# Kernel optimization log

Hardware: AMD Instinct MI355X
Metric: run time of the kernel (lower is better)

The kernel has to match this reference:

```python
import jax, jax.numpy as jnp
import numpy as np

B, S, DIN, E, M, L = 16, 4096, 64, 512, 128, 4


def _phi(u, R):
    # u: [B,S,E] (already scaled by E**-0.25), R: [E,M]
    logits = u @ R - 0.5 * jnp.sum(u * u, axis=-1, keepdims=True)
    logits = logits - jax.lax.stop_gradient(jnp.max(logits))  # constant shift cancels in num/den ratio
    return jnp.exp(logits) / np.sqrt(M).astype(np.float32)


def setup_inputs() -> dict:
    key = jax.random.key(0)
    ks = jax.random.split(key, 32)
    n = jax.random.normal
    d = {
        'x': n(ks[0], (B, S, DIN), jnp.float32),
        'Wi': n(ks[1], (DIN, E)) / np.sqrt(DIN),
        'bi': jnp.zeros((E,)),
        'pos': n(ks[2], (S, E)) * 0.02,
        'Wq': n(ks[3], (L, E, E)) / np.sqrt(E),
        'bq': jnp.zeros((L, E)),
        'Wk': n(ks[4], (L, E, E)) / np.sqrt(E),
        'bk': jnp.zeros((L, E)),
        'Wv': n(ks[5], (L, E, E)) / np.sqrt(E),
        'bv': jnp.zeros((L, E)),
        'Wo': n(ks[6], (L, E, E)) / np.sqrt(E),
        'bo': jnp.zeros((L, E)),
        'R': n(ks[7], (L, E, M)),
        'ln_g': jnp.ones((L, E)),
        'ln_b': jnp.zeros((L, E)),
        'W1': n(ks[8], (L, E, 4 * E)) / np.sqrt(E),
        'b1': jnp.zeros((L, 4 * E)),
        'W2': n(ks[9], (L, 4 * E, E)) / np.sqrt(4 * E),
        'b2': jnp.zeros((L, E)),
        'Wr1': n(ks[10], (E, E // 2)) / np.sqrt(E),
        'br1': jnp.zeros((E // 2,)),
        'Wr2': n(ks[11], (E // 2, 1)) / np.sqrt(E // 2),
        'br2': jnp.zeros((1,)),
    }
    return d


def reference(x, Wi, bi, pos, Wq, bq, Wk, bk, Wv, bv, Wo, bo, R, ln_g, ln_b, W1, b1, W2, b2, Wr1, br1, Wr2, br2):
    h = x @ Wi + bi + pos[None, :, :]  # [B,S,E]
    scale = E ** -0.25
    for i in range(L):
        residual = h
        # --- Performer linear attention (non-causal FAVOR+) ---
        q = h @ Wq[i] + bq[i]
        k = h @ Wk[i] + bk[i]
        v = h @ Wv[i] + bv[i]
        pq = _phi(q * scale, R[i])  # [B,S,M]
        pk = _phi(k * scale, R[i])  # [B,S,M]
        kv = jnp.einsum('bsm,bse->bme', pk, v)  # [B,M,E]
        z = jnp.sum(pk, axis=1)                  # [B,M]
        num = jnp.einsum('bsm,bme->bse', pq, kv)
        den = jnp.einsum('bsm,bm->bs', pq, z)[..., None]
        a = (num / (den + 1e-6)) @ Wo[i] + bo[i]
        # --- LayerNorm ---
        mu = jnp.mean(a, axis=-1, keepdims=True)
        var = jnp.var(a, axis=-1, keepdims=True)
        y = (a - mu) * jax.lax.rsqrt(var + 1e-5) * ln_g[i] + ln_b[i]
        # --- FFN (dropout is identity in eval) ---
        ff = jax.nn.gelu(y @ W1[i] + b1[i], approximate=False) @ W2[i] + b2[i]
        h = ff + residual
    pooled = h[:, 0, :]  # [B,E]
    return jax.nn.relu(pooled @ Wr1 + br1) @ Wr2 + br2  # [B,1]
```

## Files before the change

### kernel.cpp

```cpp
#include <hip/hip_runtime.h>
#include <math.h>

static constexpr int  cB   = 16;
static constexpr int  cS   = 4096;
static constexpr int  cDIN = 64;
static constexpr int  cE   = 512;
static constexpr int  cM   = 128;
static constexpr int  cL   = 4;
static constexpr int  cFF  = 2048;
static constexpr int  cHE  = 256;
static constexpr long cNBS = (long)cB * cS;
static constexpr int  cNF  = 1536;

typedef __attribute__((ext_vector_type(8))) short  bf16x8;
typedef __attribute__((ext_vector_type(4))) short  bf16x4;
typedef __attribute__((ext_vector_type(4))) float  f32x4;

typedef const __attribute__((address_space(1))) unsigned int g_u32;
typedef __attribute__((address_space(3))) unsigned int l_u32;

__device__ __forceinline__ float b2f(unsigned short u) {
  union { unsigned int i; float f; } x; x.i = ((unsigned int)u) << 16; return x.f;
}
__device__ __forceinline__ unsigned short f2b(float f) {
  union { float f; unsigned int i; } x; x.f = f;
  unsigned int r = x.i + 0x7FFFu + ((x.i >> 16) & 1u);
  return (unsigned short)(r >> 16);
}

#define PSCALE 0.21022410381342863f
#define PNRM   0.022097086912079608f
#define PINV   0.08838834764831845f

#define FLAG_BIAS    2
#define FLAG_GELU    4
#define FLAG_RES     8
#define FLAG_VT      16
#define FLAG_DEN     32
#define FLAG_RNORM   64
#define FLAG_PHIK    128
#define FLAG_F32OUT  256
#define FLAG_SPLITK8 512
#define FLAG_ATOMIC  1024
#define FLAG_FUSED   2048
#define FLAG_SWZ     4096

#define GMT 128
#define GNT 128
#define GBK 64


__global__ __launch_bounds__(256, 2)
void gemm_kernel(const unsigned short* __restrict__ A,
                 const unsigned short* __restrict__ Bt,
                 const unsigned short* __restrict__ bias,
                 const unsigned short* __restrict__ Res,
                 const float* __restrict__ aux,
                 float* __restrict__ pmax,
                 void* __restrict__ C,
                 int K, int N, int lda, int ldb, float alpha, int flags,
                 long sA, long sB, long sC)
{
  __shared__ __align__(16) unsigned char sraw[32800];
  unsigned short (*As)[64] = (unsigned short (*)[64])sraw;
  unsigned short (*Bs)[64] = (unsigned short (*)[64])(sraw + 16384);
  unsigned short (*stage)[136] = (unsigned short (*)[136])sraw;
  float* wred  = (float*)(sraw + 32768);

  const int tid  = threadIdx.x;
  const int lane = tid & 63;
  const int wid  = tid >> 6;

  int bx = blockIdx.x, by = blockIdx.y;
  if (flags & FLAG_SWZ) {
    const unsigned lid  = blockIdx.x + gridDim.x * blockIdx.y;
    const unsigned xcd  = lid & 7u;
    const unsigned slot = lid >> 3;
    bx = (int)(xcd * (gridDim.y >> 3) + slot / gridDim.x);
    by = (int)(slot % gridDim.x);
  }

  long zb = blockIdx.z;
  const long zc = blockIdx.z;
  int koff = 0;
  if (flags & FLAG_SPLITK8) { koff = (int)(zb & 7) * K; zb >>= 3; }

  const unsigned short* Ab = A + zb * sA + (long)bx * GMT * lda + koff;
  const unsigned short* Bb = Bt + zb * sB + (long)by * GNT * ldb + koff;

  const int srow  = tid >> 3;
  const int scolG = (((tid & 7) ^ (srow & 7)) << 3);
  const unsigned short* gA = Ab + (long)srow * lda + scolG;
  const unsigned short* gB = Bb + (long)srow * ldb + scolG;
  l_u32* lA = (l_u32*)(sraw + tid * 16);
  l_u32* lB = (l_u32*)(sraw + 16384 + tid * 16);

  const f32x4 fzero = {0.f, 0.f, 0.f, 0.f};
  f32x4 acc[4][4];
#pragma unroll
  for (int i = 0; i < 4; ++i)
#pragma unroll
    for (int j = 0; j < 4; ++j) acc[i][j] = fzero;

  const int wm = (wid >> 1) << 6;
  const int wn = (wid & 1) << 6;
  const int fm = lane & 15;
  const int kqh = lane >> 4;

  const long ka32 = (long)32 * lda, kb32 = (long)32 * ldb;
  for (int k0 = 0; k0 < K; k0 += GBK) {
#pragma unroll
    for (int s = 0; s < 4; ++s) {
      __builtin_amdgcn_global_load_lds((g_u32*)(gA + (long)s * ka32 + k0),
                                       (l_u32*)((__attribute__((address_space(3))) char*)lA + s * 4096), 16, 0, 0);
      __builtin_amdgcn_global_load_lds((g_u32*)(gB + (long)s * kb32 + k0),
                                       (l_u32*)((__attribute__((address_space(3))) char*)lB + s * 4096), 16, 0, 0);
    }
    __syncthreads();

#pragma unroll
    for (int kk = 0; kk < 2; ++kk) {
      bf16x8 af[4], bfv[4];
#pragma unroll
      for (int i = 0; i < 4; ++i) {
        const int ca = ((((kk << 2) | kqh) ^ (fm & 7)) << 3);
        af[i]  = *(const bf16x8*)&As[wm + i * 16 + fm][ca];
        bfv[i] = *(const bf16x8*)&Bs[wn + i * 16 + fm][ca];
      }
#pragma unroll
      for (int i = 0; i < 4; ++i)
#pragma unroll
        for (int j = 0; j < 4; ++j)
          acc[i][j] = __builtin_amdgcn_mfma_f32_16x16x32_bf16(af[i], bfv[j], acc[i][j], 0, 0, 0);
    }
    __syncthreads();
  }

  const int rq = (lane >> 4) << 2;
  const long crow0 = (long)bx * GMT + wm;
  const int  ccol0 = by * GNT + wn;

  long rnoff = 0;
  if (flags & FLAG_FUSED) {
    if (by < 4) flags = FLAG_BIAS | FLAG_VT;
    else { flags = FLAG_BIAS | FLAG_RNORM; if (by >= 8) rnoff = cNBS; }
  }

  if (flags & FLAG_RNORM) {
#pragma unroll
    for (int i = 0; i < 4; ++i)
#pragma unroll
      for (int r = 0; r < 4; ++r) {
        float s = 0.f;
#pragma unroll
        for (int j = 0; j < 4; ++j) {
          float v = acc[i][j][r] * alpha + b2f(bias[ccol0 + j * 16 + fm]);
          s += v * v;
        }
        s += __shfl_xor(s, 1, 64);
        s += __shfl_xor(s, 2, 64);
        s += __shfl_xor(s, 4, 64);
        s += __shfl_xor(s, 8, 64);
        if (fm == 0)
          unsafeAtomicAdd(&pmax[rnoff + crow0 + i * 16 + rq + r], s);
      }
    return;
  }

  if (flags & FLAG_PHIK) {
    const long aoff = (by == 0) ? cNBS : 0;
    float* Cf = (float*)C + (long)by * (cNBS * (long)cM);
    float mx = -3.0e38f;
#pragma unroll
    for (int i = 0; i < 4; ++i)
#pragma unroll
      for (int r = 0; r < 4; ++r) {
        const long rr = crow0 + i * 16 + rq + r;
        const float nrm = PNRM * aux[aoff + rr];
#pragma unroll
        for (int j = 0; j < 4; ++j) {
          const int cc = ccol0 + j * 16 + fm;
          const float bv = b2f(bias[cc]);
          float l = acc[i][j][r] * PSCALE + bv - nrm;
          mx = fmaxf(mx, l);
          Cf[rr * (long)cM + (cc & (cM - 1))] = l;
        }
      }
#pragma unroll
    for (int off = 32; off >= 1; off >>= 1) mx = fmaxf(mx, __shfl_down(mx, off, 64));
    if (lane == 0) wred[wid] = mx;
    __syncthreads();
    if (tid == 0)
      pmax[by * 512 + bx] = fmaxf(fmaxf(wred[0], wred[1]), fmaxf(wred[2], wred[3]));
    return;
  }

  if (flags & FLAG_ATOMIC) {
    float* Cf = (float*)C + zb * sC;
#pragma unroll
    for (int j = 0; j < 4; ++j) {
      const int cc = ccol0 + j * 16 + fm;
#pragma unroll
      for (int i = 0; i < 4; ++i)
#pragma unroll
        for (int r = 0; r < 4; ++r) {
          const long rr = crow0 + i * 16 + rq + r;
          unsafeAtomicAdd(&Cf[rr * (long)N + cc], acc[i][j][r] * alpha);
        }
    }
    return;
  }

  if (flags & FLAG_VT) {
    unsigned short* Cb = (unsigned short*)C;
    const int bb = (bx * GMT) >> 12;
    const long sbase = (long)((bx * GMT) & (cS - 1));
#pragma unroll
    for (int rnd = 0; rnd < 2; ++rnd) {
      if ((wn >> 6) == rnd) {
#pragma unroll
        for (int j = 0; j < 4; ++j) {
          const int cc = ccol0 + j * 16 + fm;
          const float bv = (flags & FLAG_BIAS) ? b2f(bias[cc]) : 0.f;
          const int cl = j * 16 + fm;
#pragma unroll
          for (int i = 0; i < 4; ++i)
#pragma unroll
            for (int r = 0; r < 4; ++r)
              stage[cl][wm + i * 16 + rq + r] = f2b(acc[i][j][r] * alpha + bv);
        }
      }
      __syncthreads();
      {
        const int cl = tid >> 2;
        const int sseg = (tid & 3) << 5;
        const int gcol = by * GNT + rnd * 64 + cl;
        unsigned short* dst = Cb + (long)bb * sC + (long)gcol * cS + sbase + sseg;
#pragma unroll
        for (int t = 0; t < 4; ++t)
          *(bf16x8*)(dst + t * 8) = *(const bf16x8*)&stage[cl][sseg + t * 8];
      }
      __syncthreads();
    }
    return;
  }

  const long rowsPerBatch = (long)gridDim.x * GMT;
#pragma unroll
  for (int j = 0; j < 4; ++j) {
    const int cc = ccol0 + j * 16 + fm;
    const float bv = (flags & FLAG_BIAS) ? b2f(bias[cc]) : 0.f;
#pragma unroll
    for (int i = 0; i < 4; ++i) {
      const long rbase = crow0 + i * 16 + rq;
#pragma unroll
      for (int r = 0; r < 4; ++r) {
        const long rr = rbase + r;
        float v = acc[i][j][r] * alpha;
        if (flags & FLAG_DEN)
          v *= 1.f / (fmaxf(aux[zb * rowsPerBatch + rr], 0.f) + 1e-6f);
        v += bv;
        if (flags & FLAG_GELU) v = 0.5f * v * (1.f + erff(v * 0.7071067811865475f));
        const long idx = zc * sC + rr * (long)N + cc;
        if (flags & FLAG_RES) v += b2f(Res[idx]);
        if (flags & FLAG_F32OUT) ((float*)C)[idx] = v;
        else                     ((unsigned short*)C)[idx] = f2b(v);
      }
    }
  }
}

__global__ void detect_kernel(const unsigned short* __restrict__ lng,
                              int* __restrict__ flag) {
  if (threadIdx.x == 0 && blockIdx.x == 0) flag[0] = (lng[0] == 0) ? 1 : 0;
}

__global__ __launch_bounds__(256) void cvt_kernel(const void* __restrict__ in,
                                                  unsigned short* __restrict__ out,
                                                  long n, const int* __restrict__ flag) {
  long i = (long)blockIdx.x * 256 + threadIdx.x;
  if (i >= n) return;
  if (flag[0]) out[i] = f2b(((const float*)in)[i]);
  else         out[i] = ((const unsigned short*)in)[i];
}

__global__ __launch_bounds__(256) void zero4_kernel(float* __restrict__ p) {
  long i = ((long)blockIdx.x * 256 + threadIdx.x) * 4;
  f32x4 z = {0.f, 0.f, 0.f, 0.f};
  *(f32x4*)&p[i] = z;
}

__global__ __launch_bounds__(256) void addpos_kernel(unsigned short* __restrict__ h,
                                                     const unsigned short* __restrict__ pos) {
  long i = ((long)blockIdx.x * 256 + threadIdx.x) * 8;
  long se = i % ((long)cS * cE);
  bf16x8 v = *(bf16x8*)&h[i];
  bf16x8 p = *(const bf16x8*)&pos[se];
#pragma unroll
  for (int r = 0; r < 8; ++r)
    v[r] = (short)f2b(b2f((unsigned short)v[r]) + b2f((unsigned short)p[r]));
  *(bf16x8*)&h[i] = v;
}

__global__ __launch_bounds__(256) void reducemax2_kernel(const float* __restrict__ partials,
                                                         float* __restrict__ gmax) {
  __shared__ float sm[8];
  const int tid = threadIdx.x;
  for (int half = 0; half < 2; ++half) {
    float mx = -3.0e38f;
    for (int i = tid; i < 512; i += 256) mx = fmaxf(mx, partials[half * 512 + i]);
#pragma unroll
    for (int off = 32; off >= 1; off >>= 1) mx = fmaxf(mx, __shfl_down(mx, off, 64));
    if ((tid & 63) == 0) sm[(half << 2) + (tid >> 6)] = mx;
  }
  __syncthreads();
  if (tid == 0) gmax[0] = fmaxf(fmaxf(sm[0], sm[1]), fmaxf(sm[2], sm[3]));
  if (tid == 1) gmax[1] = fmaxf(fmaxf(sm[4], sm[5]), fmaxf(sm[6], sm[7]));
}

__global__ __launch_bounds__(256) void expq_kernel(const float* __restrict__ lf,
                                                   const float* __restrict__ gmx,
                                                   unsigned short* __restrict__ P) {
  long i = ((long)blockIdx.x * 256 + threadIdx.x) * 4;
  const float gm = gmx[0];
  f32x4 v = *(const f32x4*)&lf[i];
  bf16x4 o;
#pragma unroll
  for (int r = 0; r < 4; ++r)
    o[r] = (short)f2b(__expf(fminf(v[r] - gm, 0.f)) * PINV);
  *(bf16x4*)&P[i] = o;
}

__global__ __launch_bounds__(256) void expT_kernel(const float* __restrict__ lf,
                                                   const float* __restrict__ gmx,
                                                   unsigned short* __restrict__ out) {
  __shared__ unsigned short t[32][33];
  const int b = blockIdx.z;
  const float gm = gmx[0];
  const int bx = blockIdx.x << 5, by = blockIdx.y << 5;
  const int tx = threadIdx.x & 31, ty = threadIdx.x >> 5;
  const float* src = lf + (long)b * cS * cM;
  unsigned short* dst = out + (long)b * cM * cS;
#pragma unroll
  for (int i = ty; i < 32; i += 8) {
    float l = src[(long)(by + i) * cM + bx + tx];
    t[i][tx] = f2b(__expf(fminf(l - gm, 0.f)) * PINV);
  }
  __syncthreads();
#pragma unroll
  for (int i = ty; i < 32; i += 8)
    dst[(long)(bx + i) * cS + by + tx] = t[tx][i];
}

__global__ __launch_bounds__(256) void kvcvt_kernel(const float* __restrict__ kvacc,
                                                    unsigned short* __restrict__ kvtb) {
  long i = ((long)blockIdx.x * 256 + threadIdx.x) * 4;
  f32x4 v = *(const f32x4*)&kvacc[i];
  bf16x4 o;
#pragma unroll
  for (int r = 0; r < 4; ++r) o[r] = (short)f2b(v[r]);
  *(bf16x4*)&kvtb[i] = o;
}

__global__ __launch_bounds__(128) void phibias_kernel(const unsigned short* __restrict__ bq,
                                                      const unsigned short* __restrict__ R,
                                                      unsigned short* __restrict__ out,
                                                      float scale, int ldo) {
  const int l = blockIdx.x, m = threadIdx.x;
  const unsigned short* b = bq + (long)l * cE;
  const unsigned short* r = R + (long)l * cE * cM;
  float a = 0.f;
  for (int e = 0; e < cE; ++e) a += b2f(b[e]) * b2f(r[(long)e * cM + m]);
  out[(long)l * ldo + m] = f2b(a * scale);
}

__global__ __launch_bounds__(256) void packb_kernel(const unsigned short* __restrict__ bv,
                                                    const unsigned short* __restrict__ bk,
                                                    const unsigned short* __restrict__ bq,
                                                    unsigned short* __restrict__ out) {
  const int l = blockIdx.x, t = threadIdx.x;
#pragma unroll
  for (int s = 0; s < 512; s += 256) {
    out[l * cNF + s + t]        = bv[l * 512 + s + t];
    out[l * cNF + 512 + s + t]  = bk[l * 512 + s + t];
    out[l * cNF + 1024 + s + t] = bq[l * 512 + s + t];
  }
}

__global__ __launch_bounds__(256) void zsumt_kernel(const unsigned short* __restrict__ qtb,
                                                    float* __restrict__ z) {
  __shared__ float sred[4];
  const int b = blockIdx.x, m = blockIdx.y, tid = threadIdx.x;
  const unsigned short* p = qtb + ((long)b * cM + m) * cS + (long)tid * 16;
  bf16x8 a = *(const bf16x8*)p;
  bf16x8 c = *(const bf16x8*)(p + 8);
  float s = 0.f;
#pragma unroll
  for (int t = 0; t < 8; ++t) s += b2f((unsigned short)a[t]) + b2f((unsigned short)c[t]);
#pragma unroll
  for (int off = 32; off >= 1; off >>= 1) s += __shfl_down(s, off, 64);
  const int w = tid >> 6, lane = tid & 63;
  if (lane == 0) sred[w] = s;
  __syncthreads();
  if (tid == 0) z[b * cM + m] = sred[0] + sred[1] + sred[2] + sred[3];
}

__global__ __launch_bounds__(256) void den_kernel(const unsigned short* __restrict__ P,
                                                  const float* __restrict__ z,
                                                  float* __restrict__ den) {
  const int w = threadIdx.x >> 6, lane = threadIdx.x & 63;
  const long row = (long)blockIdx.x * 4 + w;
  const float* zb = z + (row >> 12) * cM;
  const unsigned short* p = P + row * cM;
  float d = b2f(p[lane]) * zb[lane] + b2f(p[lane + 64]) * zb[lane + 64];
#pragma unroll
  for (int off = 32; off >= 1; off >>= 1) d += __shfl_down(d, off, 64);
  if (lane == 0) den[row] = d;
}

__global__ __launch_bounds__(256) void ln_kernel(unsigned short* __restrict__ a,
                                                 const unsigned short* __restrict__ g,
                                                 const unsigned short* __restrict__ bb) {
  __shared__ float sred[8];
  const long row = blockIdx.x;
  unsigned short* ar = a + row * cE;
  const int tid = threadIdx.x;
  float v0 = b2f(ar[tid]), v1 = b2f(ar[tid + 256]);
  float s = v0 + v1, sq = v0 * v0 + v1 * v1;
#pragma unroll
  for (int off = 32; off >= 1; off >>= 1) {
    s  += __shfl_down(s, off, 64);
    sq += __shfl_down(sq, off, 64);
  }
  const int w = tid >> 6, lane = tid & 63;
  if (lane == 0) { sred[w] = s; sred[4 + w] = sq; }
  __syncthreads();
  const float st  = sred[0] + sred[1] + sred[2] + sred[3];
  const float sqt = sred[4] + sred[5] + sred[6] + sred[7];
  const float mean = st * (1.f / 512.f);
  const float var  = fmaxf(sqt * (1.f / 512.f) - mean * mean, 0.f);
  const float rstd = rsqrtf(var + 1e-5f);
  ar[tid]       = f2b((v0 - mean) * rstd * b2f(g[tid])       + b2f(bb[tid]));
  ar[tid + 256] = f2b((v1 - mean) * rstd * b2f(g[tid + 256]) + b2f(bb[tid + 256]));
}

__global__ __launch_bounds__(256) void transpose_kernel(const unsigned short* __restrict__ in,
                                                        unsigned short* __restrict__ out,
                                                        int R, int C, long sIn, long sOut) {
  __shared__ unsigned short t[32][33];
  in  += (long)blockIdx.z * sIn;
  out += (long)blockIdx.z * sOut;
  const int bx = blockIdx.x << 5, by = blockIdx.y << 5;
  const int tx = threadIdx.x & 31, ty = threadIdx.x >> 5;
#pragma unroll
  for (int i = ty; i < 32; i += 8) t[i][tx] = in[(long)(by + i) * C + bx + tx];
  __syncthreads();
#pragma unroll
  for (int i = ty; i < 32; i += 8) out[(long)(bx + i) * R + by + tx] = t[tx][i];
}

__global__ __launch_bounds__(256) void head_kernel(const unsigned short* __restrict__ h,
                                                   const unsigned short* __restrict__ Wr1,
                                                   const unsigned short* __restrict__ br1,
                                                   const unsigned short* __restrict__ Wr2,
                                                   const unsigned short* __restrict__ br2,
                                                   void* __restrict__ out,
                                                   const int* __restrict__ flag) {
  __shared__ float pooled[cE];
  __shared__ float red[4];
  const int b = blockIdx.x, tid = threadIdx.x;
  pooled[tid]       = b2f(h[(long)b * cS * cE + tid]);
  pooled[tid + 256] = b2f(h[(long)b * cS * cE + tid + 256]);
  __syncthreads();
  float acc = b2f(br1[tid]);
  for (int e = 0; e < cE; ++e) acc += pooled[e] * b2f(Wr1[e * cHE + tid]);
  acc = fmaxf(acc, 0.f) * b2f(Wr2[tid]);
#pragma unroll
  for (int off = 32; off >= 1; off >>= 1) acc += __shfl_down(acc, off, 64);
  const int w = tid >> 6, lane = tid & 63;
  if (lane == 0) red[w] = acc;
  __syncthreads();
  if (tid == 0) {
    float r = red[0] + red[1] + red[2] + red[3] + b2f(br2[0]);
    if (flag[0]) ((float*)out)[b] = r;
    else         ((unsigned short*)out)[b] = f2b(r);
  }
}

extern "C" void kernel_launch(void* const* d_in, const int* in_sizes, int n_in,
                              void* d_out, int out_size, void* d_ws, size_t ws_size,
                              hipStream_t stream) {
  (void)in_sizes; (void)n_in; (void)out_size;

  char* ws = (char*)d_ws;
  size_t off = 0;
  auto alloc = [&](size_t bytes) -> void* {
    void* p = ws + off;
    off += (bytes + 255) & ~(size_t)255;
    return p;
  };
  unsigned short* h   = (unsigned short*)alloc(cNBS * cE * 2);
  unsigned short* X   = (unsigned short*)alloc(cNBS * cE * 2);
  unsigned short* Y   = (unsigned short*)alloc(cNBS * cE * 2);
  unsigned short* Pb  = (unsigned short*)alloc(cNBS * cM * 2);
  unsigned short* kvtb= (unsigned short*)alloc((long)cB * cM * cE * 2);
  unsigned short* kvotb=(unsigned short*)alloc((long)cB * cE * cM * 2);
  float* kvacc        = (float*)alloc((long)cB * cM * cE * 4);
  float* vec64k       = (float*)alloc(cNBS * 4);
  float* rnorm2       = (float*)alloc(2 * cNBS * 4);
  float* z            = (float*)alloc(cB * cM * 4);
  float* partials     = (float*)alloc(1024 * 4);
  float* gmaxf        = (float*)alloc(256);
  int*   dflag        = (int*)alloc(256);
  unsigned short* WiT = (unsigned short*)alloc((long)cE * cDIN * 2);
  unsigned short* BigB= (unsigned short*)alloc((long)cL * cNF * cE * 2);
  unsigned short* BigL= (unsigned short*)alloc((long)cL * 256 * cE * 2);
  unsigned short* WoT = (unsigned short*)alloc((long)cL * cE * cE * 2);
  unsigned short* RT  = (unsigned short*)alloc((long)cL * cM * cE * 2);
  unsigned short* W1T = (unsigned short*)alloc((long)cL * cFF * cE * 2);
  unsigned short* W2T = (unsigned short*)alloc((long)cL * cE * cFF * 2);
  unsigned short* sb  = (unsigned short*)alloc(170000 * 2);

  unsigned short* WqB = X;
  unsigned short* WkB = WqB + (long)cL * cE * cE;
  unsigned short* WvB = WkB + (long)cL * cE * cE;
  unsigned short* WoB = WvB + (long)cL * cE * cE;
  unsigned short* RmB = WoB + (long)cL * cE * cE;
  unsigned short* W1B = RmB + (long)cL * cE * cM;
  unsigned short* W2B = W1B + (long)cL * cE * cFF;
  unsigned short* WiB = W2B + (long)cL * cE * cFF;
  unsigned short* xb   = Y;
  unsigned short* posb = Y + cNBS * cDIN;
  unsigned short* biC  = sb;
  unsigned short* bqC  = biC  + 512;
  unsigned short* bkC  = bqC  + 2048;
  unsigned short* bvC  = bkC  + 2048;
  unsigned short* boC  = bvC  + 2048;
  unsigned short* b1C  = boC  + 2048;
  unsigned short* b2C  = b1C  + 8192;
  unsigned short* lngC = b2C  + 2048;
  unsigned short* lnbC = lngC + 2048;
  unsigned short* Wr1C = lnbC + 2048;
  unsigned short* br1C = Wr1C + 131072;
  unsigned short* Wr2C = br1C + 256;
  unsigned short* br2C = Wr2C + 256;
  unsigned short* bqkC  = br2C + 16;
  unsigned short* b1536C = bqkC + cL * 256;

  unsigned short* qtb  = X;
  float* logfX         = (float*)X;
  unsigned short* vtb  = Y;
  unsigned short* ab   = Y;
  unsigned short* u1b  = X;

  if (off > ws_size) return;

  detect_kernel<<<1, 64, 0, stream>>>((const unsigned short*)d_in[13], dflag);
  auto cvt = [&](const void* src, unsigned short* dst, long n) {
    cvt_kernel<<<(unsigned)((n + 255) / 256), 256, 0, stream>>>(src, dst, n, dflag);
  };
  cvt(d_in[0],  xb,   cNBS * cDIN);
  cvt(d_in[1],  WiB,  (long)cDIN * cE);
  cvt(d_in[2],  biC,  cE);
  cvt(d_in[3],  posb, (long)cS * cE);
  cvt(d_in[4],  WqB,  (long)cL * cE * cE);
  cvt(d_in[5],  bqC,  (long)cL * cE);
  cvt(d_in[6],  WkB,  (long)cL * cE * cE);
  cvt(d_in[7],  bkC,  (long)cL * cE);
  cvt(d_in[8],  WvB,  (long)cL * cE * cE);
  cvt(d_in[9],  bvC,  (long)cL * cE);
  cvt(d_in[10], WoB,  (long)cL * cE * cE);
  cvt(d_in[11], boC,  (long)cL * cE);
  cvt(d_in[12], RmB,  (long)cL * cE * cM);
  cvt(d_in[13], lngC, (long)cL * cE);
  cvt(d_in[14], lnbC, (long)cL * cE);
  cvt(d_in[15], W1B,  (long)cL * cE * cFF);
  cvt(d_in[16], b1C,  (long)cL * cFF);
  cvt(d_in[17], W2B,  (long)cL * cFF * cE);
  cvt(d_in[18], b2C,  (long)cL * cE);
  cvt(d_in[19], Wr1C, (long)cE * cHE);
  cvt(d_in[20], br1C, cHE);
  cvt(d_in[21], Wr2C, cHE);
  cvt(d_in[22], br2C, 1);

  typedef const unsigned short* cus;
  auto gemm = [&](const void* A, const void* Bt, const void* bias_,
                  const float* aux_, float* pmax_, void* C,
                  long rows, int K, int N, int lda, int ldb, float alpha, int flags,
                  long sA, long sB, long sC, int batches, const void* Res_ = nullptr) {
    dim3 g((unsigned)(rows / 128), (unsigned)(N / 128), (unsigned)batches);
    gemm_kernel<<<g, dim3(256), 0, stream>>>(
        (const unsigned short*)A, (const unsigned short*)Bt,
        (const unsigned short*)bias_, (const unsigned short*)Res_,
        aux_, pmax_, C, K, N, lda, ldb, alpha, flags, sA, sB, sC);
  };

  transpose_kernel<<<dim3(16, 2, 1), 256, 0, stream>>>(WiB, WiT, cDIN, cE, 0, 0);
  transpose_kernel<<<dim3(16, 16, cL), 256, 0, stream>>>(WvB, BigB, cE, cE, (long)cE * cE, (long)cNF * cE);
  transpose_kernel<<<dim3(16, 16, cL), 256, 0, stream>>>(WkB, BigB + (long)512 * cE, cE, cE, (long)cE * cE, (long)cNF * cE);
  transpose_kernel<<<dim3(16, 16, cL), 256, 0, stream>>>(WqB, BigB + (long)1024 * cE, cE, cE, (long)cE * cE, (long)cNF * cE);
  transpose_kernel<<<dim3(16, 16, cL), 256, 0, stream>>>(WoB, WoT, cE, cE, (long)cE * cE, (long)cE * cE);
  transpose_kernel<<<dim3(4, 16, cL), 256, 0, stream>>>(RmB, RT, cE, cM, (long)cE * cM, (long)cE * cM);
  transpose_kernel<<<dim3(64, 16, cL), 256, 0, stream>>>(W1B, W1T, cE, cFF, (long)cE * cFF, (long)cE * cFF);
  transpose_kernel<<<dim3(16, 64, cL), 256, 0, stream>>>(W2B, W2T, cFF, cE, (long)cFF * cE, (long)cFF * cE);

  gemm(RT, WqB, nullptr, nullptr, nullptr, BigL, cM, cE, cE, cE, cE, 1.f, 0,
       (long)cM * cE, (long)cE * cE, (long)256 * cE, cL);
  gemm(RT, WkB, nullptr, nullptr, nullptr, BigL + (long)128 * cE, cM, cE, cE, cE, cE, 1.f, 0,
       (long)cM * cE, (long)cE * cE, (long)256 * cE, cL);
  phibias_kernel<<<cL, 128, 0, stream>>>(bqC, RmB, bqkC, PSCALE, 256);
  phibias_kernel<<<cL, 128, 0, stream>>>(bkC, RmB, bqkC + 128, PSCALE, 256);
  packb_kernel<<<cL, 256, 0, stream>>>(bvC, bkC, bqC, b1536C);

  gemm(xb, WiT, biC, nullptr, nullptr, h, cNBS, cDIN, cE, cDIN, cDIN, 1.f,
       FLAG_BIAS, 0, 0, 0, 1);
  addpos_kernel<<<16384, 256, 0, stream>>>(h, posb);

  for (int i = 0; i < cL; ++i) {
    cus WoT_i = WoT + (long)i * cE * cE;  cus bo_i = boC + (long)i * cE;
    cus BigB_i = BigB + (long)i * cNF * cE;
    cus BigL_i = BigL + (long)i * 256 * cE;
    cus b1536_i = b1536C + (long)i * cNF;
    cus bqk_i = bqkC + (long)i * 256;
    cus g_i   = lngC + (long)i * cE;      cus b_i  = lnbC + (long)i * cE;
    cus W1T_i = W1T + (long)i * cFF * cE; cus b1_i = b1C + (long)i * cFF;
    cus W2T_i = W2T + (long)i * cE * cFF; cus b2_i = b2C + (long)i * cE;

    zero4_kernel<<<128, 256, 0, stream>>>(rnorm2);
    gemm_kernel<<<dim3(12, 512, 1), dim3(256), 0, stream>>>(
        h, BigB_i, b1536_i, nullptr, nullptr, rnorm2, vtb,
        cE, cNF, cE, cE, 1.f, FLAG_FUSED | FLAG_SWZ, 0, 0, (long)cE * cS);

    gemm_kernel<<<dim3(2, 512, 1), dim3(256), 0, stream>>>(
        h, BigL_i, bqk_i, nullptr, rnorm2, partials, logfX,
        cE, 256, cE, cE, PSCALE, FLAG_PHIK | FLAG_BIAS | FLAG_SWZ, 0, 0, 0);

    reducemax2_kernel<<<1, 256, 0, stream>>>(partials, gmaxf);
    expq_kernel<<<8192, 256, 0, stream>>>(logfX, gmaxf, Pb);
    expT_kernel<<<dim3(4, 128, cB), 256, 0, stream>>>(logfX + cNBS * cM, gmaxf + 1, qtb);

    zsumt_kernel<<<dim3(cB, cM), 256, 0, stream>>>(qtb, z);
    den_kernel<<<16384, 256, 0, stream>>>(Pb, z, vec64k);

    zero4_kernel<<<1024, 256, 0, stream>>>(kvacc);
    gemm(qtb, vtb, nullptr, nullptr, nullptr, kvacc, cM, cS / 8, cE, cS, cS, 1.f,
         FLAG_SPLITK8 | FLAG_ATOMIC, (long)cM * cS, (long)cE * cS, (long)cM * cE, cB * 8);
    kvcvt_kernel<<<1024, 256, 0, stream>>>(kvacc, kvtb);

    gemm(WoT_i, kvtb, nullptr, nullptr, nullptr, kvotb, cE, cE, cM, cE, cE, 1.f,
         0, 0, (long)cM * cE, (long)cE * cM, cB);

    gemm(Pb, kvotb, bo_i, vec64k, nullptr, ab, cS, cM, cE, cM, cM, 1.f,
         FLAG_DEN | FLAG_BIAS, (long)cS * cM, (long)cE * cM, (long)cS * cE, cB);
    ln_kernel<<<cNBS, 256, 0, stream>>>(ab, g_i, b_i);

    for (int c = 0; c < 4; ++c) {
      const unsigned short* yc = ab + (long)c * 16384 * cE;
      unsigned short* hc = h + (long)c * 16384 * cE;
      gemm_kernel<<<dim3(16, 128, 1), dim3(256), 0, stream>>>(
          yc, W1T_i, b1_i, nullptr, nullptr, nullptr, u1b,
          cE, cFF, cE, cE, 1.f, FLAG_BIAS | FLAG_GELU | FLAG_SWZ, 0, 0, 0);
      gemm_kernel<<<dim3(4, 128, 1), dim3(256), 0, stream>>>(
          u1b, W2T_i, b2_i, hc, nullptr, nullptr, hc,
          cFF, cE, cFF, cFF, 1.f, FLAG_BIAS | FLAG_RES | FLAG_SWZ, 0, 0, 0);
    }
  }

  head_kernel<<<cB, 256, 0, stream>>>(h, Wr1C, br1C, Wr2C, br2C, d_out, dflag);
}
```

Measured before the change: 3.714 ms.

## Fold phi logit projection into fused QKV GEMM, defer norm subtraction

Measured after the change: 3.624 ms. 2.4% less time.

```diff
diff --git a/kernel.cpp b/kernel.cpp
--- a/kernel.cpp
+++ b/kernel.cpp
@@ -10,7 +10,7 @@
 static constexpr int  cFF  = 2048;
 static constexpr int  cHE  = 256;
 static constexpr long cNBS = (long)cB * cS;
-static constexpr int  cNF  = 1536;
+static constexpr int  cNF  = 1792;
 
 typedef __attribute__((ext_vector_type(8))) short  bf16x8;
 typedef __attribute__((ext_vector_type(4))) short  bf16x4;
@@ -38,7 +38,6 @@
 #define FLAG_VT      16
 #define FLAG_DEN     32
 #define FLAG_RNORM   64
-#define FLAG_PHIK    128
 #define FLAG_F32OUT  256
 #define FLAG_SPLITK8 512
 #define FLAG_ATOMIC  1024
@@ -61,11 +60,10 @@
                  int K, int N, int lda, int ldb, float alpha, int flags,
                  long sA, long sB, long sC)
 {
-  __shared__ __align__(16) unsigned char sraw[32800];
+  __shared__ __align__(16) unsigned char sraw[32768];
   unsigned short (*As)[64] = (unsigned short (*)[64])sraw;
   unsigned short (*Bs)[64] = (unsigned short (*)[64])(sraw + 16384);
   unsigned short (*stage)[136] = (unsigned short (*)[136])sraw;
-  float* wred  = (float*)(sraw + 32768);
 
   const int tid  = threadIdx.x;
   const int lane = tid & 63;
@@ -142,6 +140,30 @@
 
   long rnoff = 0;
   if (flags & FLAG_FUSED) {
+    if (by >= 12) {
+      float* Lf  = (float*)Res + (long)(by - 12) * (cNBS * (long)cM);
+      float* rmx = (float*)aux + ((long)(by - 12) * 2 + (wn >> 6)) * cNBS;
+#pragma unroll
+      for (int i = 0; i < 4; ++i)
+#pragma unroll
+        for (int r = 0; r < 4; ++r) {
+          const long rr = crow0 + i * 16 + rq + r;
+          float mx = -3.0e38f;
+#pragma unroll
+          for (int j = 0; j < 4; ++j) {
+            const int cc = ccol0 + j * 16 + fm;
+            float l = acc[i][j][r] * PSCALE + b2f(bias[cc]);
+            mx = fmaxf(mx, l);
+            Lf[rr * (long)cM + (cc & (cM - 1))] = l;
+          }
+          mx = fmaxf(mx, __shfl_xor(mx, 1, 64));
+          mx = fmaxf(mx, __shfl_xor(mx, 2, 64));
+          mx = fmaxf(mx, __shfl_xor(mx, 4, 64));
+          mx = fmaxf(mx, __shfl_xor(mx, 8, 64));
+          if (fm == 0) rmx[rr] = mx;
+        }
+      return;
+    }
     if (by < 4) flags = FLAG_BIAS | FLAG_VT;
     else { flags = FLAG_BIAS | FLAG_RNORM; if (by >= 8) rnoff = cNBS; }
   }
@@ -164,34 +186,6 @@
         if (fm == 0)
           unsafeAtomicAdd(&pmax[rnoff + crow0 + i * 16 + rq + r], s);
       }
-    return;
-  }
-
-  if (flags & FLAG_PHIK) {
-    const long aoff = (by == 0) ? cNBS : 0;
-    float* Cf = (float*)C + (long)by * (cNBS * (long)cM);
-    float mx = -3.0e38f;
-#pragma unroll
-    for (int i = 0; i < 4; ++i)
-#pragma unroll
-      for (int r = 0; r < 4; ++r) {
-        const long rr = crow0 + i * 16 + rq + r;
-        const float nrm = PNRM * aux[aoff + rr];
-#pragma unroll
-        for (int j = 0; j < 4; ++j) {
-          const int cc = ccol0 + j * 16 + fm;
-          const float bv = b2f(bias[cc]);
-          float l = acc[i][j][r] * PSCALE + bv - nrm;
-          mx = fmaxf(mx, l);
-          Cf[rr * (long)cM + (cc & (cM - 1))] = l;
-        }
-      }
-#pragma unroll
-    for (int off = 32; off >= 1; off >>= 1) mx = fmaxf(mx, __shfl_down(mx, off, 64));
-    if (lane == 0) wred[wid] = mx;
-    __syncthreads();
-    if (tid == 0)
-      pmax[by * 512 + bx] = fmaxf(fmaxf(wred[0], wred[1]), fmaxf(wred[2], wred[3]));
     return;
   }
 
@@ -302,13 +296,31 @@
   *(bf16x8*)&h[i] = v;
 }
 
+__global__ __launch_bounds__(256) void reduceg_kernel(const float* __restrict__ rmax,
+                                                      const float* __restrict__ rnorm2,
+                                                      float* __restrict__ partials) {
+  __shared__ float sm[4];
+  const int b = blockIdx.x;
+  const int side = b >> 8;
+  const long row = ((long)(b & 255)) * 256 + threadIdx.x;
+  const float nrm = PNRM * rnorm2[(side == 0 ? cNBS : 0) + row];
+  float v = fmaxf(rmax[((long)side * 2 + 0) * cNBS + row],
+                  rmax[((long)side * 2 + 1) * cNBS + row]) - nrm;
+#pragma unroll
+  for (int off = 32; off >= 1; off >>= 1) v = fmaxf(v, __shfl_down(v, off, 64));
+  const int w = threadIdx.x >> 6, lane = threadIdx.x & 63;
+  if (lane == 0) sm[w] = v;
+  __syncthreads();
+  if (threadIdx.x == 0)
+    partials[b] = fmaxf(fmaxf(sm[0], sm[1]), fmaxf(sm[2], sm[3]));
+}
+
 __global__ __launch_bounds__(256) void reducemax2_kernel(const float* __restrict__ partials,
                                                          float* __restrict__ gmax) {
   __shared__ float sm[8];
   const int tid = threadIdx.x;
   for (int half = 0; half < 2; ++half) {
-    float mx = -3.0e38f;
-    for (int i = tid; i < 512; i += 256) mx = fmaxf(mx, partials[half * 512 + i]);
+    float mx = partials[half * 256 + tid];
 #pragma unroll
     for (int off = 32; off >= 1; off >>= 1) mx = fmaxf(mx, __shfl_down(mx, off, 64));
     if ((tid & 63) == 0) sm[(half << 2) + (tid >> 6)] = mx;
@@ -320,19 +332,22 @@
 
 __global__ __launch_bounds__(256) void expq_kernel(const float* __restrict__ lf,
                                                    const float* __restrict__ gmx,
+                                                   const float* __restrict__ rn,
                                                    unsigned short* __restrict__ P) {
   long i = ((long)blockIdx.x * 256 + threadIdx.x) * 4;
   const float gm = gmx[0];
+  const float nrm = PNRM * rn[i >> 7];
   f32x4 v = *(const f32x4*)&lf[i];
   bf16x4 o;
 #pragma unroll
   for (int r = 0; r < 4; ++r)
-    o[r] = (short)f2b(__expf(fminf(v[r] - gm, 0.f)) * PINV);
+    o[r] = (short)f2b(__expf(fminf(v[r] - nrm - gm, 0.f)) * PINV);
   *(bf16x4*)&P[i] = o;
 }
 
 __global__ __launch_bounds__(256) void expT_kernel(const float* __restrict__ lf,
                                                    const float* __restrict__ gmx,
+                                                   const float* __restrict__ rn,
                                                    unsigned short* __restrict__ out) {
   __shared__ unsigned short t[32][33];
   const int b = blockIdx.z;
@@ -343,8 +358,9 @@
   unsigned short* dst = out + (long)b * cM * cS;
 #pragma unroll
   for (int i = ty; i < 32; i += 8) {
+    const float nrm = PNRM * rn[(long)b * cS + by + i];
     float l = src[(long)(by + i) * cM + bx + tx];
-    t[i][tx] = f2b(__expf(fminf(l - gm, 0.f)) * PINV);
+    t[i][tx] = f2b(__expf(fminf(l - nrm - gm, 0.f)) * PINV);
   }
   __syncthreads();
 #pragma unroll
@@ -377,6 +393,7 @@
 __global__ __launch_bounds__(256) void packb_kernel(const unsigned short* __restrict__ bv,
                                                     const unsigned short* __restrict__ bk,
                                                     const unsigned short* __restrict__ bq,
+                                                    const unsigned short* __restrict__ sqk,
                                                     unsigned short* __restrict__ out) {
   const int l = blockIdx.x, t = threadIdx.x;
 #pragma unroll
@@ -385,6 +402,7 @@
     out[l * cNF + 512 + s + t]  = bk[l * 512 + s + t];
     out[l * cNF + 1024 + s + t] = bq[l * 512 + s + t];
   }
+  out[l * cNF + 1536 + t] = sqk[l * 256 + t];
 }
 
 __global__ __launch_bounds__(256) void zsumt_kernel(const unsigned short* __restrict__ qtb,
@@ -508,13 +526,13 @@
   float* kvacc        = (float*)alloc((long)cB * cM * cE * 4);
   float* vec64k       = (float*)alloc(cNBS * 4);
   float* rnorm2       = (float*)alloc(2 * cNBS * 4);
+  float* rmax         = (float*)alloc(4 * cNBS * 4);
   float* z            = (float*)alloc(cB * cM * 4);
   float* partials     = (float*)alloc(1024 * 4);
   float* gmaxf        = (float*)alloc(256);
   int*   dflag        = (int*)alloc(256);
   unsigned short* WiT = (unsigned short*)alloc((long)cE * cDIN * 2);
   unsigned short* BigB= (unsigned short*)alloc((long)cL * cNF * cE * 2);
-  unsigned short* BigL= (unsigned short*)alloc((long)cL * 256 * cE * 2);
   unsigned short* WoT = (unsigned short*)alloc((long)cL * cE * cE * 2);
   unsigned short* RT  = (unsigned short*)alloc((long)cL * cM * cE * 2);
   unsigned short* W1T = (unsigned short*)alloc((long)cL * cFF * cE * 2);
@@ -545,7 +563,7 @@
   unsigned short* Wr2C = br1C + 256;
   unsigned short* br2C = Wr2C + 256;
   unsigned short* bqkC  = br2C + 16;
-  unsigned short* b1536C = bqkC + cL * 256;
+  unsigned short* b1792C = bqkC + cL * 256;
 
   unsigned short* qtb  = X;
   float* logfX         = (float*)X;
@@ -604,13 +622,13 @@
   transpose_kernel<<<dim3(64, 16, cL), 256, 0, stream>>>(W1B, W1T, cE, cFF, (long)cE * cFF, (long)cE * cFF);
   transpose_kernel<<<dim3(16, 64, cL), 256, 0, stream>>>(W2B, W2T, cFF, cE, (long)cFF * cE, (long)cFF * cE);
 
-  gemm(RT, WqB, nullptr, nullptr, nullptr, BigL, cM, cE, cE, cE, cE, 1.f, 0,
-       (long)cM * cE, (long)cE * cE, (long)256 * cE, cL);
-  gemm(RT, WkB, nullptr, nullptr, nullptr, BigL + (long)128 * cE, cM, cE, cE, cE, cE, 1.f, 0,
-       (long)cM * cE, (long)cE * cE, (long)256 * cE, cL);
+  gemm(RT, WqB, nullptr, nullptr, nullptr, BigB + (long)1536 * cE, cM, cE, cE, cE, cE, 1.f, 0,
+       (long)cM * cE, (long)cE * cE, (long)cNF * cE, cL);
+  gemm(RT, WkB, nullptr, nullptr, nullptr, BigB + (long)1664 * cE, cM, cE, cE, cE, cE, 1.f, 0,
+       (long)cM * cE, (long)cE * cE, (long)cNF * cE, cL);
   phibias_kernel<<<cL, 128, 0, stream>>>(bqC, RmB, bqkC, PSCALE, 256);
   phibias_kernel<<<cL, 128, 0, stream>>>(bkC, RmB, bqkC + 128, PSCALE, 256);
-  packb_kernel<<<cL, 256, 0, stream>>>(bvC, bkC, bqC, b1536C);
+  packb_kernel<<<cL, 256, 0, stream>>>(bvC, bkC, bqC, bqkC, b1792C);
 
   gemm(xb, WiT, biC, nullptr, nullptr, h, cNBS, cDIN, cE, cDIN, cDIN, 1.f,
        FLAG_BIAS, 0, 0, 0, 1);
@@ -619,25 +637,21 @@
   for (int i = 0; i < cL; ++i) {
     cus WoT_i = WoT + (long)i * cE * cE;  cus bo_i = boC + (long)i * cE;
     cus BigB_i = BigB + (long)i * cNF * cE;
-    cus BigL_i = BigL + (long)i * 256 * cE;
-    cus b1536_i = b1536C + (long)i * cNF;
-    cus bqk_i = bqkC + (long)i * 256;
+    cus b1792_i = b1792C + (long)i * cNF;
     cus g_i   = lngC + (long)i * cE;      cus b_i  = lnbC + (long)i * cE;
     cus W1T_i = W1T + (long)i * cFF * cE; cus b1_i = b1C + (long)i * cFF;
     cus W2T_i = W2T + (long)i * cE * cFF; cus b2_i = b2C + (long)i * cE;
 
     zero4_kernel<<<128, 256, 0, stream>>>(rnorm2);
-    gemm_kernel<<<dim3(12, 512, 1), dim3(256), 0, stream>>>(
-        h, BigB_i, b1536_i, nullptr, nullptr, rnorm2, vtb,
-        cE, cNF, cE, cE, 1.f, FLAG_FUSED | FLAG_SWZ, 0, 0, (long)cE * cS);
-
-    gemm_kernel<<<dim3(2, 512, 1), dim3(256), 0, stream>>>(
-        h, BigL_i, bqk_i, nullptr, rnorm2, partials, logfX,
-        cE, 256, cE, cE, PSCALE, FLAG_PHIK | FLAG_BIAS | FLAG_SWZ, 0, 0, 0);
-
+    gemm_kernel<<<dim3(14, 512, 1), dim3(256), 0, stream>>>(
+        h, BigB_i, b1792_i, (const unsigned short*)logfX, (const float*)rmax,
+        rnorm2, vtb, cE, cNF, cE, cE, 1.f, FLAG_FUSED | FLAG_SWZ,
+        0, 0, (long)cE * cS);
+
+    reduceg_kernel<<<512, 256, 0, stream>>>(rmax, rnorm2, partials);
     reducemax2_kernel<<<1, 256, 0, stream>>>(partials, gmaxf);
-    expq_kernel<<<8192, 256, 0, stream>>>(logfX, gmaxf, Pb);
-    expT_kernel<<<dim3(4, 128, cB), 256, 0, stream>>>(logfX + cNBS * cM, gmaxf + 1, qtb);
+    expq_kernel<<<8192, 256, 0, stream>>>(logfX, gmaxf, rnorm2 + cNBS, Pb);
+    expT_kernel<<<dim3(4, 128, cB), 256, 0, stream>>>(logfX + cNBS * cM, gmaxf + 1, rnorm2, qtb);
 
     zsumt_kernel<<<dim3(cB, cM), 256, 0, stream>>>(qtb, z);
     den_kernel<<<16384, 256, 0, stream>>>(Pb, z, vec64k);
```
